# Kernel optimization log

Hardware: AMD Instinct MI355X
Metric: run time of the kernel (lower is better)

Reference implementation:

```python
import jax, jax.numpy as jnp
import numpy as np
from jax import lax

B, C_IN, T = 64, 40, 8192

def conv1d(x, w, b):
    # x: [B,C,T], w: [O,I,K] (torch Conv1d layout), stride 2, VALID padding
    y = lax.conv_general_dilated(x, w, window_strides=(2,), padding='VALID',
                                 dimension_numbers=('NCH', 'OIH', 'NCH'))
    return y + b[None, :, None]

def avgpool2(x):
    # AvgPool1d(kernel=2, stride=2): pairwise mean, drop trailing odd element
    t2 = x.shape[-1] // 2
    return x[..., :2 * t2].reshape(x.shape[0], x.shape[1], t2, 2).mean(-1)

def setup_inputs():
    key = jax.random.key(0)
    ks = jax.random.split(key, 24)
    def w_init(k, shape, fan_in):
        return jax.random.normal(k, shape, jnp.float32) * (1.0 / np.sqrt(fan_in))
    inp = {}
    inp['x_input'] = jax.random.normal(ks[0], (B, C_IN, T), jnp.float32)
    # per-sample valid lengths in [2048, 8192] so the deep strided stack leaves >=1 frame
    inp['len_mask'] = 2048 + jax.random.randint(ks[1], (B,), 0, T - 2048 + 1, dtype=jnp.int32)
    convs = [(96, C_IN, 10), (96, 96, 5), (96, 96, 5), (96, 96, 5), (96, 96, 5), (96, 96, 5), (128, 96, 3)]
    for i, (o, ci, k) in enumerate(convs):
        inp[f'w{i+1}'] = w_init(ks[2 + 2 * i], (o, ci, k), ci * k)
        inp[f'b{i+1}'] = jnp.zeros((o,), jnp.float32)
    lins = [(128, 128), (64, 128), (5, 64)]
    for i, (o, ci) in enumerate(lins):
        inp[f'lw{i+1}'] = w_init(ks[16 + 2 * i], (o, ci), ci)
        inp[f'lb{i+1}'] = jnp.zeros((o,), jnp.float32)
    return inp

def reference(x_input, len_mask, w1, b1, w2, b2, w3, b3, w4, b4, w5, b5, w6, b6, w7, b7,
              lw1, lb1, lw2, lb2, lw3, lb3):
    # Batched masked equivalent of the per-sample ragged loop: for VALID stride-2 convs,
    # output position j depends only on inputs < valid length when j < valid out-length,
    # so we run batched convs on padded input and track per-sample valid lengths.
    Lv = len_mask.astype(jnp.int32)
    x = jax.nn.relu(conv1d(x_input, w1, b1)); Lv = (Lv - 10) // 2 + 1
    x = jax.nn.relu(conv1d(x, w2, b2));       Lv = (Lv - 5) // 2 + 1
    x = jax.nn.relu(conv1d(x, w3, b3));       Lv = (Lv - 5) // 2 + 1
    # cnn_1d_top (dropout in eval mode = identity)
    x = conv1d(x, w4, b4);        Lv = (Lv - 5) // 2 + 1
    x = jax.nn.relu(avgpool2(x)); Lv = Lv // 2
    x = conv1d(x, w5, b5);        Lv = (Lv - 5) // 2 + 1
    x = jax.nn.relu(avgpool2(x)); Lv = Lv // 2
    x = jax.nn.relu(conv1d(x, w6, b6)); Lv = (Lv - 5) // 2 + 1
    x = jax.nn.relu(conv1d(x, w7, b7)); Lv = (Lv - 3) // 2 + 1
    # AdaptiveMaxPool1d(1) over each sample's valid region
    mask = jnp.arange(x.shape[-1])[None, :] < Lv[:, None]          # [B, T_out]
    x = jnp.max(jnp.where(mask[:, None, :], x, -jnp.inf), axis=-1)  # [B, 128]
    # out1_top MLP head
    h = jax.nn.relu(x @ lw1.T + lb1)
    h = jax.nn.relu(h @ lw2.T + lb2)
    return h @ lw3.T + lb3
```

## Files before the change

### kernel.cpp

```cpp
#include <hip/hip_runtime.h>
#include <hip/hip_bf16.h>
#include <math.h>


typedef __attribute__((ext_vector_type(8))) _Float16 f16x8;
typedef __attribute__((ext_vector_type(4))) float f32x4;

__device__ __forceinline__ unsigned short f2h_bits(float f) {
    union { _Float16 h; unsigned short u; } cv;
    cv.h = (_Float16)f;
    return cv.u;
}

__device__ __forceinline__ void stage16(const void* g, void* l) {
    __builtin_amdgcn_global_load_lds(
        (const __attribute__((address_space(1))) unsigned int*)g,
        (__attribute__((address_space(3))) unsigned int*)l, 16, 0, 0);
}

template<int KEFF, int KW, int CI, int NBLK, bool IN_FP32, bool RELU, bool OUT_F16, bool POOL>
__global__ __launch_bounds__(256)
void conv_tight(const unsigned short* __restrict__ xh,
                const unsigned short* __restrict__ wpk,
                const float* __restrict__ bias,
                unsigned short* __restrict__ yh,
                float* __restrict__ yf,
                int Tin, int Tout)
{
    constexpr int CO    = 96;
    constexpr int GTOT  = CI * KEFF;
    constexpr int STEPS = (GTOT + 31) / 32;
    constexpr int NR    = (KEFF + 29) / KEFF + 1;
    constexpr int RD    = NBLK + KEFF / 2;
    constexpr int NTW   = NBLK / 64;
    constexpr int TOT   = NR * RD;
    constexpr int NIT   = (TOT + 255) / 256;

    __shared__ __align__(16) unsigned short As[2][6144];
    __shared__ unsigned int Bs[2][TOT];

    const int tid  = threadIdx.x;
    const int lane = tid & 63;
    const int wave = tid >> 6;
    const int quad = lane >> 4;
    const int l16  = lane & 15;
    const int wc0  = wave * (NBLK / 4);

    const int nT = (Tout + NBLK - 1) / NBLK;
    const int b  = blockIdx.x / nT;
    const int t0 = (blockIdx.x % nT) * NBLK;

    const float* xf = (const float*)xh;
    const unsigned int* xb = (const unsigned int*)xh + (((size_t)b * CI * Tin) >> 1);
    const int rowd = Tin >> 1;

    auto stageA = [&](int s, int bufi) {
        const char* g = (const char*)(wpk + (size_t)s * 6144) + (size_t)lane * 16;
        char* l = (char*)&As[bufi][0] + (size_t)lane * 16;
        #pragma unroll
        for (int i = 0; i < 3; ++i) {
            int seg = i * 4 + wave;
            stage16(g + seg * 1024, l + seg * 1024);
        }
    };

    unsigned int breg[NIT];
    auto loadB = [&](int s) {
        const int cb = (32 * s) / KEFF;
        #pragma unroll
        for (int it = 0; it < NIT; ++it) {
            int i = tid + it * 256;
            if (i < TOT) {
                int r = i / RD, d = i - r * RD;
                int ci = cb + r;
                if (ci > CI - 1) ci = CI - 1;
                if (IN_FP32) {
                    int e = 2 * (t0 + d);
                    if (e > Tin - 2) e = Tin - 2;
                    const float* src = xf + ((size_t)b * CI + ci) * Tin + e;
                    float2 v = *(const float2*)src;
                    breg[it] = (unsigned int)f2h_bits(v.x)
                             | ((unsigned int)f2h_bits(v.y) << 16);
                } else {
                    breg[it] = *(xb + (size_t)ci * rowd + t0 + d);
                }
            }
        }
    };
    auto storeB = [&](int bufi) {
        #pragma unroll
        for (int it = 0; it < NIT; ++it) {
            int i = tid + it * 256;
            if (i < TOT) Bs[bufi][i] = breg[it];
        }
    };

    f32x4 acc[6][NTW];
    #pragma unroll
    for (int mt = 0; mt < 6; ++mt)
        #pragma unroll
        for (int nt = 0; nt < NTW; ++nt) acc[mt][nt] = (f32x4)0.f;

    loadB(0); storeB(0); stageA(0, 0);
    __syncthreads();

    #pragma unroll
    for (int s = 0; s < STEPS; ++s) {
        const int buf = s & 1;

        if (s + 1 < STEPS) {
            loadB(s + 1);
            stageA(s + 1, buf ^ 1);
        }

        f16x8 Ah[6], Al[6];
        #pragma unroll
        for (int mt = 0; mt < 6; ++mt) {
            Ah[mt] = *(const f16x8*)&As[buf][(mt) * 512 + lane * 8];
            Al[mt] = *(const f16x8*)&As[buf][(6 + mt) * 512 + lane * 8];
        }

        const int cb = (32 * s) / KEFF;
        int offp[4];
        #pragma unroll
        for (int p = 0; p < 4; ++p) {
            unsigned g = (unsigned)(32 * s + quad * 8 + 2 * p);
            unsigned ci = g / (unsigned)KEFF;
            unsigned dwo = (g - ci * (unsigned)KEFF) >> 1;
            offp[p] = ((int)ci - cb) * RD + wc0 + l16 + (int)dwo;
        }

        #pragma unroll
        for (int nt = 0; nt < NTW; ++nt) {
            union { unsigned int u[4]; f16x8 v; } Bv;
            #pragma unroll
            for (int p = 0; p < 4; ++p) Bv.u[p] = Bs[buf][offp[p] + nt * 16];
            #pragma unroll
            for (int mt = 0; mt < 6; ++mt)
                acc[mt][nt] = __builtin_amdgcn_mfma_f32_16x16x32_f16(Ah[mt], Bv.v, acc[mt][nt], 0, 0, 0);
            #pragma unroll
            for (int mt = 0; mt < 6; ++mt)
                acc[mt][nt] = __builtin_amdgcn_mfma_f32_16x16x32_f16(Al[mt], Bv.v, acc[mt][nt], 0, 0, 0);
        }

        if (s + 1 < STEPS) storeB(buf ^ 1);
        __syncthreads();
    }

    #pragma unroll
    for (int mt = 0; mt < 6; ++mt) {
        #pragma unroll
        for (int r = 0; r < 4; ++r) {
            int o = mt * 16 + quad * 4 + r;
            float bv = bias[o];
            #pragma unroll
            for (int nt = 0; nt < NTW; ++nt) {
                int t = t0 + wc0 + nt * 16 + l16;
                float v = acc[mt][nt][r] + bv;
                if (RELU) v = fmaxf(v, 0.f);
                if (POOL) {
                    float sum = v + __shfl_xor(v, 1, 64);
                    if ((lane & 1) == 0 && t + 1 < Tout) {
                        float pr = fmaxf(0.5f * sum, 0.f);
                        size_t pidx = ((size_t)b * CO + o) * (Tout >> 1) + (t >> 1);
                        if (OUT_F16) yh[pidx] = f2h_bits(pr);
                        else         yf[pidx] = pr;
                    }
                } else if (t < Tout) {
                    size_t oidx = ((size_t)b * CO + o) * Tout + t;
                    if (OUT_F16) yh[oidx] = f2h_bits(v);
                    else         yf[oidx] = v;
                }
            }
        }
    }
}

__device__ __forceinline__ void repack_img(const float* __restrict__ w,
                                           unsigned short* __restrict__ wpk,
                                           int idx, int KP, int KW, int CI)
{
    int j = idx & 7, lane = (idx >> 3) & 63, g = idx >> 9;
    int c = g / 24, r = g % 24;
    int mt = r % 6, sh = r / 6;
    int half = sh & 1, s = sh >> 1;
    int S  = c * 2 + s;
    int kg = S * 32 + (lane >> 4) * 8 + j;
    int o  = mt * 16 + (lane & 15);
    int ci = kg / KP, k = kg - ci * KP;
    float val = (ci < CI && k < KW) ? w[((size_t)o * CI + ci) * KW + k] : 0.f;
    _Float16 hh = (_Float16)val;
    union { _Float16 h; unsigned short u; } cv;
    cv.h = (half == 0) ? hh : (_Float16)(val - (float)hh);
    wpk[idx] = cv.u;
}
__device__ __forceinline__ void repack_okc(const float* __restrict__ w,
                                           float* __restrict__ wr,
                                           int idx, int CI, int K, int CO)
{
    int o = idx % CO; int rem = idx / CO; int k = rem % K; int ci = rem / K;
    wr[idx] = w[((size_t)o * CI + ci) * K + k];
}

__global__ void repack_all(const float* w1, const float* w2, const float* w3,
                           const float* w4, const float* w5, const float* w6,
                           const float* w7,
                           unsigned short* p1, unsigned short* p2,
                           unsigned short* p3, unsigned short* p4,
                           unsigned short* p5, float* r6, float* r7)
{
    int idx = blockIdx.x * 256 + threadIdx.x;
    if (idx < 79872)  { repack_img(w1, p1, idx, 10, 10, 40); return; }
    idx -= 79872;
    if (idx < 110592) { repack_img(w2, p2, idx, 6, 5, 96); return; }
    idx -= 110592;
    if (idx < 110592) { repack_img(w3, p3, idx, 6, 5, 96); return; }
    idx -= 110592;
    if (idx < 110592) { repack_img(w4, p4, idx, 6, 5, 96); return; }
    idx -= 110592;
    if (idx < 110592) { repack_img(w5, p5, idx, 6, 5, 96); return; }
    idx -= 110592;
    if (idx < 46080)  { repack_okc(w6, r6, idx, 96, 5, 96); return; }
    idx -= 46080;
    if (idx < 36864)  { repack_okc(w7, r7, idx, 96, 3, 128); return; }
}

__global__ __launch_bounds__(256)
void conv6_k(const float* __restrict__ y5p, const float* __restrict__ w6r,
             const float* __restrict__ b6, float* __restrict__ y6)
{
    __shared__ float s5[96 * 62];
    const int b = blockIdx.x >> 2, ob = blockIdx.x & 3;
    const int tid = threadIdx.x;
    for (int i = tid; i < 96 * 62; i += 256) s5[i] = y5p[(size_t)b * 96 * 62 + i];
    __syncthreads();

    const int wave = __builtin_amdgcn_readfirstlane(tid >> 6);
    const int t = tid & 63;
    if (t < 29) {
        const int o0 = ob * 24 + wave * 6;
        float a[6];
        #pragma unroll
        for (int oo = 0; oo < 6; oo++) a[oo] = 0.f;
        for (int ci = 0; ci < 96; ci++) {
            float xr[5];
            #pragma unroll
            for (int k = 0; k < 5; k++) xr[k] = s5[ci * 62 + 2 * t + k];
            #pragma unroll
            for (int k = 0; k < 5; k++) {
                const float* wp = w6r + (ci * 5 + k) * 96 + o0;
                #pragma unroll
                for (int oo = 0; oo < 6; oo++)
                    a[oo] = fmaf(wp[oo], xr[k], a[oo]);
            }
        }
        #pragma unroll
        for (int oo = 0; oo < 6; oo++)
            y6[((size_t)b * 96 + o0 + oo) * 29 + t] = fmaxf(a[oo] + b6[o0 + oo], 0.f);
    }
}

__global__ __launch_bounds__(256)
void tail2(const float* __restrict__ y6,
           const float* __restrict__ w7r, const float* __restrict__ b7,
           const int* __restrict__ lens,
           const float* __restrict__ lw1, const float* __restrict__ lb1,
           const float* __restrict__ lw2, const float* __restrict__ lb2,
           const float* __restrict__ lw3, const float* __restrict__ lb3,
           float* __restrict__ out)
{
    __shared__ float s6[96 * 29 + 8];
    __shared__ float s7[128 * 14];
    __shared__ float feat[128], h1[128], h2[64];

    const int b = blockIdx.x, tid = threadIdx.x;
    for (int i = tid; i < 96 * 29; i += 256) s6[i] = y6[(size_t)b * 96 * 29 + i];
    __syncthreads();

    const int wave = __builtin_amdgcn_readfirstlane(tid >> 6);
    const int lane = tid & 63;
    const int sub  = lane >> 4;
    const int tl   = lane & 15;
    {
        float a[32];
        #pragma unroll
        for (int oo = 0; oo < 32; oo++) a[oo] = 0.f;
        const int ci0 = sub * 24;
        for (int ci = ci0; ci < ci0 + 24; ci++) {
            float xr[3];
            #pragma unroll
            for (int k = 0; k < 3; k++) xr[k] = s6[ci * 29 + 2 * tl + k];
            #pragma unroll
            for (int k = 0; k < 3; k++) {
                const float* wp = w7r + (ci * 3 + k) * 128 + wave * 32;
                #pragma unroll
                for (int oo = 0; oo < 32; oo++)
                    a[oo] = fmaf(wp[oo], xr[k], a[oo]);
            }
        }
        #pragma unroll
        for (int oo = 0; oo < 32; oo++) {
            float v = a[oo];
            v += __shfl_xor(v, 16, 64);
            v += __shfl_xor(v, 32, 64);
            if (sub == 0 && tl < 14) {
                int o = wave * 32 + oo;
                s7[o * 14 + tl] = fmaxf(v + b7[o], 0.f);
            }
        }
    }
    __syncthreads();

    if (tid < 128) {
        int L = lens[b];
        L = (L - 10) / 2 + 1;
        L = (L - 5) / 2 + 1;
        L = (L - 5) / 2 + 1;
        L = (L - 5) / 2 + 1;
        L = L / 2;
        L = (L - 5) / 2 + 1;
        L = L / 2;
        L = (L - 5) / 2 + 1;
        L = (L - 3) / 2 + 1;
        float m = -INFINITY;
        for (int t = 0; t < L; t++) m = fmaxf(m, s7[tid * 14 + t]);
        feat[tid] = m;
    }
    __syncthreads();

    if (tid < 128) {
        float s = lb1[tid];
        for (int i = 0; i < 128; i++) s = fmaf(lw1[tid * 128 + i], feat[i], s);
        h1[tid] = fmaxf(s, 0.f);
    }
    __syncthreads();
    if (tid < 64) {
        float s = lb2[tid];
        for (int i = 0; i < 128; i++) s = fmaf(lw2[tid * 128 + i], h1[i], s);
        h2[tid] = fmaxf(s, 0.f);
    }
    __syncthreads();
    if (tid < 5) {
        float s = lb3[tid];
        for (int i = 0; i < 64; i++) s = fmaf(lw3[tid * 64 + i], h2[i], s);
        out[b * 5 + tid] = s;
    }
}

extern "C" void kernel_launch(void* const* d_in, const int* in_sizes, int n_in,
                              void* d_out, int out_size, void* d_ws, size_t ws_size,
                              hipStream_t stream)
{
    const float* x    = (const float*)d_in[0];
    const int*   lens = (const int*)  d_in[1];
    const float* w1 = (const float*)d_in[2];   const float* b1 = (const float*)d_in[3];
    const float* w2 = (const float*)d_in[4];   const float* b2 = (const float*)d_in[5];
    const float* w3 = (const float*)d_in[6];   const float* b3 = (const float*)d_in[7];
    const float* w4 = (const float*)d_in[8];   const float* b4 = (const float*)d_in[9];
    const float* w5 = (const float*)d_in[10];  const float* b5 = (const float*)d_in[11];
    const float* w6 = (const float*)d_in[12];  const float* b6 = (const float*)d_in[13];
    const float* w7 = (const float*)d_in[14];  const float* b7 = (const float*)d_in[15];
    const float* lw1 = (const float*)d_in[16]; const float* lb1 = (const float*)d_in[17];
    const float* lw2 = (const float*)d_in[18]; const float* lb2 = (const float*)d_in[19];
    const float* lw3 = (const float*)d_in[20]; const float* lb3 = (const float*)d_in[21];
    float* out = (float*)d_out;
    char*  W   = (char*)d_ws;

    size_t off = 0;
    auto take = [&](size_t bytes) {
        size_t o = off; off = (off + bytes + 255) & ~(size_t)255; return o;
    };
    size_t o_y3h = take(((size_t)64 * 96 * 1020 + 2048) * 2);
    size_t o_y4h = take(((size_t)64 * 96 * 254 + 2048) * 2);
    size_t o_y5p = take((size_t)64 * 96 * 62 * 4 + 1024);
    size_t o_y6  = take((size_t)64 * 96 * 29 * 4);
    size_t o_wp1 = take((size_t)79872 * 2);
    size_t o_wp2 = take((size_t)110592 * 2);
    size_t o_wp3 = take((size_t)110592 * 2);
    size_t o_wp4 = take((size_t)110592 * 2);
    size_t o_wp5 = take((size_t)110592 * 2);
    size_t o_w6r = take((size_t)46080 * 4);
    size_t o_w7r = take((size_t)36864 * 4);
    size_t persist = off;

    auto chunk_bytes = [&](int Bc) -> size_t {
        size_t s = 0;
        s += ((size_t)Bc * 96 * 4092 + 2048) * 2 + 256;
        s += ((size_t)Bc * 96 * 2044 + 2048) * 2 + 256;
        return s;
    };
    int Bc = 64;
    while (Bc > 1 && persist + chunk_bytes(Bc) > ws_size) Bc >>= 1;
    size_t o_y1h = take(((size_t)Bc * 96 * 4092 + 2048) * 2);
    size_t o_y2h = take(((size_t)Bc * 96 * 2044 + 2048) * 2);

    auto US = [&](size_t o) { return (unsigned short*)(W + o); };
    auto FP = [&](size_t o) { return (float*)(W + o); };

    repack_all<<<dim3((605184 + 255) / 256), 256, 0, stream>>>(
        w1, w2, w3, w4, w5, w6, w7,
        US(o_wp1), US(o_wp2), US(o_wp3), US(o_wp4), US(o_wp5),
        FP(o_w6r), FP(o_w7r));

    const int nchunks = 64 / Bc;
    for (int c = 0; c < nchunks; c++) {
        const float* xc = x + (size_t)c * Bc * 40 * 8192;

        conv_tight<10, 10, 40, 256, true, true, true, false><<<dim3(Bc * 16), 256, 0, stream>>>(
            (const unsigned short*)xc, US(o_wp1), b1, US(o_y1h), nullptr, 8192, 4092);
        conv_tight< 6, 5, 96, 256, false, true, true, false><<<dim3(Bc * 8), 256, 0, stream>>>(
            US(o_y1h), US(o_wp2), b2, US(o_y2h), nullptr, 4092, 2044);
        unsigned short* y3h_c = US(o_y3h) + (size_t)c * Bc * 96 * 1020;
        conv_tight< 6, 5, 96, 128, false, true, true, false><<<dim3(Bc * 8), 256, 0, stream>>>(
            US(o_y2h), US(o_wp3), b3, y3h_c, nullptr, 2044, 1020);
    }

    conv_tight<6, 5, 96, 128, false, false, true, true><<<dim3(64 * 4), 256, 0, stream>>>(
        US(o_y3h), US(o_wp4), b4, US(o_y4h), nullptr, 1020, 508);

    conv_tight<6, 5, 96, 64, false, false, false, true><<<dim3(64 * 2), 256, 0, stream>>>(
        US(o_y4h), US(o_wp5), b5, nullptr, FP(o_y5p), 254, 125);

    conv6_k<<<dim3(256), 256, 0, stream>>>(FP(o_y5p), FP(o_w6r), b6, FP(o_y6));

    tail2<<<dim3(64), 256, 0, stream>>>(
        FP(o_y6), FP(o_w7r), b7, lens, lw1, lb1, lw2, lb2, lw3, lb3, out);
}
```

Measured before the change: 443.6 us.

## Stage full input tile in LDS once and read weights directly from global

Replaces the double-buffered per-step staging of weights and input rows with a single up-front load of all input channels for the tile into shared memory, followed by one barrier. Weight fragments are read straight from global memory (relying on caches) instead of being copied into LDS with global_load_lds. This removes the per-step __syncthreads calls and the LDS traffic for weights. In exchange, the whole loop loses its load/compute overlap, shared memory use per block grows with CI, which can lower occupancy, and the second conv switches from 256 to 128 outputs per block with twice as many blocks.

```diff
diff --git a/kernel.cpp b/kernel.cpp
--- a/kernel.cpp
+++ b/kernel.cpp
@@ -12,32 +12,24 @@
     return cv.u;
 }
 
-__device__ __forceinline__ void stage16(const void* g, void* l) {
-    __builtin_amdgcn_global_load_lds(
-        (const __attribute__((address_space(1))) unsigned int*)g,
-        (__attribute__((address_space(3))) unsigned int*)l, 16, 0, 0);
-}
-
-template<int KEFF, int KW, int CI, int NBLK, bool IN_FP32, bool RELU, bool OUT_F16, bool POOL>
+template<int KEFF, int CI, int NBLK, bool IN_FP32, bool RELU, bool OUT_F16, bool POOL>
 __global__ __launch_bounds__(256)
-void conv_tight(const unsigned short* __restrict__ xh,
-                const unsigned short* __restrict__ wpk,
-                const float* __restrict__ bias,
-                unsigned short* __restrict__ yh,
-                float* __restrict__ yf,
-                int Tin, int Tout)
+void conv_nb(const unsigned short* __restrict__ xh,
+             const unsigned short* __restrict__ wpk,
+             const float* __restrict__ bias,
+             unsigned short* __restrict__ yh,
+             float* __restrict__ yf,
+             int Tin, int Tout)
 {
     constexpr int CO    = 96;
     constexpr int GTOT  = CI * KEFF;
     constexpr int STEPS = (GTOT + 31) / 32;
-    constexpr int NR    = (KEFF + 29) / KEFF + 1;
     constexpr int RD    = NBLK + KEFF / 2;
     constexpr int NTW   = NBLK / 64;
-    constexpr int TOT   = NR * RD;
+    constexpr int TOT   = CI * RD;
     constexpr int NIT   = (TOT + 255) / 256;
 
-    __shared__ __align__(16) unsigned short As[2][6144];
-    __shared__ unsigned int Bs[2][TOT];
+    __shared__ unsigned int Bs[TOT];
 
     const int tid  = threadIdx.x;
     const int lane = tid & 63;
@@ -54,46 +46,25 @@
     const unsigned int* xb = (const unsigned int*)xh + (((size_t)b * CI * Tin) >> 1);
     const int rowd = Tin >> 1;
 
-    auto stageA = [&](int s, int bufi) {
-        const char* g = (const char*)(wpk + (size_t)s * 6144) + (size_t)lane * 16;
-        char* l = (char*)&As[bufi][0] + (size_t)lane * 16;
-        #pragma unroll
-        for (int i = 0; i < 3; ++i) {
-            int seg = i * 4 + wave;
-            stage16(g + seg * 1024, l + seg * 1024);
-        }
-    };
-
-    unsigned int breg[NIT];
-    auto loadB = [&](int s) {
-        const int cb = (32 * s) / KEFF;
-        #pragma unroll
-        for (int it = 0; it < NIT; ++it) {
-            int i = tid + it * 256;
-            if (i < TOT) {
-                int r = i / RD, d = i - r * RD;
-                int ci = cb + r;
-                if (ci > CI - 1) ci = CI - 1;
-                if (IN_FP32) {
-                    int e = 2 * (t0 + d);
-                    if (e > Tin - 2) e = Tin - 2;
-                    const float* src = xf + ((size_t)b * CI + ci) * Tin + e;
-                    float2 v = *(const float2*)src;
-                    breg[it] = (unsigned int)f2h_bits(v.x)
-                             | ((unsigned int)f2h_bits(v.y) << 16);
-                } else {
-                    breg[it] = *(xb + (size_t)ci * rowd + t0 + d);
-                }
-            }
-        }
-    };
-    auto storeB = [&](int bufi) {
-        #pragma unroll
-        for (int it = 0; it < NIT; ++it) {
-            int i = tid + it * 256;
-            if (i < TOT) Bs[bufi][i] = breg[it];
-        }
-    };
+    #pragma unroll
+    for (int it = 0; it < NIT; ++it) {
+        int i = tid + it * 256;
+        if (i < TOT) {
+            int r = (unsigned)i / (unsigned)RD, d = i - r * RD;
+            unsigned int v;
+            if (IN_FP32) {
+                int e = 2 * (t0 + d);
+                if (e > Tin - 2) e = Tin - 2;
+                const float* src = xf + ((size_t)b * CI + r) * Tin + e;
+                float2 w = *(const float2*)src;
+                v = (unsigned int)f2h_bits(w.x) | ((unsigned int)f2h_bits(w.y) << 16);
+            } else {
+                v = *(xb + (size_t)r * rowd + t0 + d);
+            }
+            Bs[i] = v;
+        }
+    }
+    __syncthreads();
 
     f32x4 acc[6][NTW];
     #pragma unroll
@@ -101,50 +72,36 @@
         #pragma unroll
         for (int nt = 0; nt < NTW; ++nt) acc[mt][nt] = (f32x4)0.f;
 
-    loadB(0); storeB(0); stageA(0, 0);
-    __syncthreads();
-
     #pragma unroll
     for (int s = 0; s < STEPS; ++s) {
-        const int buf = s & 1;
-
-        if (s + 1 < STEPS) {
-            loadB(s + 1);
-            stageA(s + 1, buf ^ 1);
-        }
-
-        f16x8 Ah[6], Al[6];
+        int offp[4];
+        #pragma unroll
+        for (int p = 0; p < 4; ++p) {
+            int g = 32 * s + quad * 8 + 2 * p;
+            if (g > GTOT - 2) g = GTOT - 2;
+            unsigned ci = (unsigned)g / (unsigned)KEFF;
+            unsigned dwo = ((unsigned)g - ci * (unsigned)KEFF) >> 1;
+            offp[p] = (int)ci * RD + wc0 + l16 + (int)dwo;
+        }
+
+        union { unsigned int u[4]; f16x8 v; } Bv[NTW];
+        #pragma unroll
+        for (int nt = 0; nt < NTW; ++nt)
+            #pragma unroll
+            for (int p = 0; p < 4; ++p) Bv[nt].u[p] = Bs[offp[p] + nt * 16];
+
+        const unsigned short* ap = wpk + (size_t)s * 6144 + (size_t)lane * 8;
         #pragma unroll
         for (int mt = 0; mt < 6; ++mt) {
-            Ah[mt] = *(const f16x8*)&As[buf][(mt) * 512 + lane * 8];
-            Al[mt] = *(const f16x8*)&As[buf][(6 + mt) * 512 + lane * 8];
-        }
-
-        const int cb = (32 * s) / KEFF;
-        int offp[4];
-        #pragma unroll
-        for (int p = 0; p < 4; ++p) {
-            unsigned g = (unsigned)(32 * s + quad * 8 + 2 * p);
-            unsigned ci = g / (unsigned)KEFF;
-            unsigned dwo = (g - ci * (unsigned)KEFF) >> 1;
-            offp[p] = ((int)ci - cb) * RD + wc0 + l16 + (int)dwo;
-        }
-
-        #pragma unroll
-        for (int nt = 0; nt < NTW; ++nt) {
-            union { unsigned int u[4]; f16x8 v; } Bv;
-            #pragma unroll
-            for (int p = 0; p < 4; ++p) Bv.u[p] = Bs[buf][offp[p] + nt * 16];
-            #pragma unroll
-            for (int mt = 0; mt < 6; ++mt)
-                acc[mt][nt] = __builtin_amdgcn_mfma_f32_16x16x32_f16(Ah[mt], Bv.v, acc[mt][nt], 0, 0, 0);
-            #pragma unroll
-            for (int mt = 0; mt < 6; ++mt)
-                acc[mt][nt] = __builtin_amdgcn_mfma_f32_16x16x32_f16(Al[mt], Bv.v, acc[mt][nt], 0, 0, 0);
-        }
-
-        if (s + 1 < STEPS) storeB(buf ^ 1);
-        __syncthreads();
+            f16x8 Ah = *(const f16x8*)(ap + mt * 512);
+            f16x8 Al = *(const f16x8*)(ap + (6 + mt) * 512);
+            #pragma unroll
+            for (int nt = 0; nt < NTW; ++nt)
+                acc[mt][nt] = __builtin_amdgcn_mfma_f32_16x16x32_f16(Ah, Bv[nt].v, acc[mt][nt], 0, 0, 0);
+            #pragma unroll
+            for (int nt = 0; nt < NTW; ++nt)
+                acc[mt][nt] = __builtin_amdgcn_mfma_f32_16x16x32_f16(Al, Bv[nt].v, acc[mt][nt], 0, 0, 0);
+        }
     }
 
     #pragma unroll
@@ -406,19 +363,19 @@
     for (int c = 0; c < nchunks; c++) {
         const float* xc = x + (size_t)c * Bc * 40 * 8192;
 
-        conv_tight<10, 10, 40, 256, true, true, true, false><<<dim3(Bc * 16), 256, 0, stream>>>(
+        conv_nb<10, 40, 256, true, true, true, false><<<dim3(Bc * 16), 256, 0, stream>>>(
             (const unsigned short*)xc, US(o_wp1), b1, US(o_y1h), nullptr, 8192, 4092);
-        conv_tight< 6, 5, 96, 256, false, true, true, false><<<dim3(Bc * 8), 256, 0, stream>>>(
+        conv_nb< 6, 96, 128, false, true, true, false><<<dim3(Bc * 16), 256, 0, stream>>>(
             US(o_y1h), US(o_wp2), b2, US(o_y2h), nullptr, 4092, 2044);
         unsigned short* y3h_c = US(o_y3h) + (size_t)c * Bc * 96 * 1020;
-        conv_tight< 6, 5, 96, 128, false, true, true, false><<<dim3(Bc * 8), 256, 0, stream>>>(
+        conv_nb< 6, 96, 128, false, true, true, false><<<dim3(Bc * 8), 256, 0, stream>>>(
             US(o_y2h), US(o_wp3), b3, y3h_c, nullptr, 2044, 1020);
     }
 
-    conv_tight<6, 5, 96, 128, false, false, true, true><<<dim3(64 * 4), 256, 0, stream>>>(
+    conv_nb<6, 96, 128, false, false, true, true><<<dim3(64 * 4), 256, 0, stream>>>(
         US(o_y3h), US(o_wp4), b4, US(o_y4h), nullptr, 1020, 508);
 
-    conv_tight<6, 5, 96, 64, false, false, false, true><<<dim3(64 * 2), 256, 0, stream>>>(
+    conv_nb<6, 96, 64, false, false, false, true><<<dim3(64 * 2), 256, 0, stream>>>(
         US(o_y4h), US(o_wp5), b5, nullptr, FP(o_y5p), 254, 125);
 
     conv6_k<<<dim3(256), 256, 0, stream>>>(FP(o_y5p), FP(o_w6r), b6, FP(o_y6));
```

Result: slower. 476.3 us (+7.4%).
